# Optimization experiments

Measured on AMD Instinct MI355X. Metric: run time of the kernel, lower is better.

The kernel has to match this reference:

```python
import jax, jax.numpy as jnp
import numpy as np

N = 4096            # number of graph nodes (keypoints)
L_MAX = 6
Q = 2
D, H, W = 64, 128, 128
ST = 0.15           # sigma_transition
SP = 0.3            # sigma_pairwise
AU = 1.0            # alpha_unary
L = len(range(0, 2 * L_MAX + 1, Q)) ** 3   # 343 displacement labels


def setup_inputs() -> dict:
    key = jax.random.key(0)
    k1, k2 = jax.random.split(key)
    unary = jax.random.normal(k1, (N, L), dtype=jnp.float32)
    u = jax.random.uniform(k2, (N, N), dtype=jnp.float32)
    dist = (u + u.T) * 0.5  # symmetric pairwise distance matrix
    # Buffer A exactly as in __init__: displacement grid -> RBF transition kernel
    r = np.arange(0, 2 * L_MAX + 1, Q, dtype=np.float32)
    g = np.stack(np.meshgrid(r, r, r, indexing='ij'), axis=3).reshape(-1, 3) - L_MAX
    disp = g[:, ::-1] * 2.0 / np.array([W - 1, H - 1, D - 1], dtype=np.float32)
    A = np.exp(-((disp[:, None, :] - disp[None, :, :]) ** 2).sum(-1) / (2.0 * ST ** 2))
    return {"unary": unary, "dist": dist, "A": jnp.asarray(A, dtype=jnp.float32)}


def _forward(unary, dist, A):
    n, l = unary.shape
    unary = AU * unary
    pairwise = jnp.exp(-dist / (2.0 * SP ** 2))
    INF = jnp.float32(1e30)
    idx = jnp.arange(n)
    d = dist.at[idx, idx].set(INF)  # no self edges

    # ---- Prim's MST rooted at node 0 (addition order = parents-before-children) ----
    in_tree0 = jnp.zeros((n,), dtype=bool).at[0].set(True)
    best0 = d[0]                      # cheapest edge from each node into the tree
    parent0 = jnp.zeros((n,), jnp.int32)
    order0 = jnp.zeros((n,), jnp.int32)

    def prim_body(i, st):
        in_tree, best, parent, order = st
        nxt = jnp.argmin(jnp.where(in_tree, INF, best)).astype(jnp.int32)
        in_tree = in_tree.at[nxt].set(True)
        order = order.at[i].set(nxt)
        upd = (d[nxt] < best) & ~in_tree
        parent = jnp.where(upd, nxt, parent)
        best = jnp.where(upd, d[nxt], best)
        return (in_tree, best, parent, order)

    _, _, parent, order = jax.lax.fori_loop(1, n, prim_body, (in_tree0, best0, parent0, order0))
    root = order[0]  # == 0

    # ---- Upward (leaves -> root) max-sum Viterbi messages along tree edges ----
    ptr0 = jnp.zeros((n, l), jnp.int32)

    def up(carry, c):
        belief, ptr = carry
        p = parent[c]
        # scores[l_c, l_p] = belief[c, l_c] + pairwise(c,p) * A[l_c, l_p]
        scores = belief[c][:, None] + pairwise[c, p] * A
        msg = scores.max(axis=0)                                   # [L]
        ptr = ptr.at[c].set(jnp.argmax(scores, axis=0).astype(jnp.int32))
        belief = belief.at[p].add(jnp.where(c == root, 0.0, msg))  # root sends nothing
        return (belief, ptr), None

    (belief, ptr), _ = jax.lax.scan(up, (unary, ptr0), order[::-1])

    # ---- Downward backtracking (root -> leaves) ----
    def down(labels, c):
        lab = jnp.where(c == root,
                        jnp.argmax(belief[root]).astype(jnp.int32),
                        ptr[c, labels[parent[c]]])
        return labels.at[c].set(lab), None

    labels, _ = jax.lax.scan(down, jnp.zeros((n,), jnp.int32), order)

    # disp_out = -1 everywhere, +1 at selected label, scaled by 1e5
    onehot = jax.nn.one_hot(labels, l, dtype=unary.dtype)
    return (2.0 * onehot - 1.0) * 100000.0


def reference(unary, dist, A):
    return _forward(unary, dist, A)
```

## Files before the change

### kernel.cpp

```cpp
#include <hip/hip_runtime.h>
#include <hip/hip_cooperative_groups.h>
#include <math.h>

namespace cg = cooperative_groups;
typedef unsigned long long u64;

#define NN 4096
#define LBL 343
#define PSTRIDE 344
#define U64MAX 0xFFFFFFFFFFFFFFFFull
#define MST_ROUNDS 12

__global__ void mrf_mst_init_kernel(int* __restrict__ compA,
                                    u64* __restrict__ minEa, u64* __restrict__ minEb,
                                    int* __restrict__ counters)
{
  const int i = blockIdx.x * blockDim.x + threadIdx.x;
  if (i < NN) { compA[i] = i; minEa[i] = U64MAX; minEb[i] = U64MAX; }
  if (i == 0) { counters[0] = NN; counters[1] = NN; counters[2] = 0; }
}

__global__ __launch_bounds__(1024) void mrf_scan_kernel(
    const float* __restrict__ dist, const int* __restrict__ compR,
    u64* __restrict__ minE, int* __restrict__ counters, int round)
{
  __shared__ int s_cc[16];
  __shared__ u64 s_cv[16];

  if (blockIdx.x == 0 && threadIdx.x == 0) counters[round & 1] = 0;
  if (round > 0 && counters[(round - 1) & 1] <= 1) return;

  const int i    = (blockIdx.x * 1024 + threadIdx.x) >> 6;
  const int lane = threadIdx.x & 63;
  const int wib  = threadIdx.x >> 6;

  const int ci = compR[i];
  const float4* rowp = (const float4*)(dist + (size_t)i * NN);
  const int4* cp = (const int4*)compR;
  u64 best = U64MAX;
  #pragma unroll 4
  for (int k = 0; k < 16; ++k) {
    const int q = k * 64 + lane;
    const float4 dv = rowp[q];
    const int4 cv = cp[q];
    const int j0 = q * 4;
    if (cv.x != ci) { const u64 p = ((u64)__float_as_uint(dv.x) << 24) | ((u64)i << 12) | (u64)(j0    ); best = best < p ? best : p; }
    if (cv.y != ci) { const u64 p = ((u64)__float_as_uint(dv.y) << 24) | ((u64)i << 12) | (u64)(j0 + 1); best = best < p ? best : p; }
    if (cv.z != ci) { const u64 p = ((u64)__float_as_uint(dv.z) << 24) | ((u64)i << 12) | (u64)(j0 + 2); best = best < p ? best : p; }
    if (cv.w != ci) { const u64 p = ((u64)__float_as_uint(dv.w) << 24) | ((u64)i << 12) | (u64)(j0 + 3); best = best < p ? best : p; }
  }
  #pragma unroll
  for (int sh = 32; sh >= 1; sh >>= 1) {
    const u64 o = __shfl_down(best, sh);
    best = best < o ? best : o;
  }
  if (lane == 0) {
    s_cc[wib] = (best == U64MAX) ? -1 : ci;
    s_cv[wib] = best;
  }
  __syncthreads();
  if (threadIdx.x == 0) {
    for (int a = 0; a < 16; ++a) {
      const int c = s_cc[a];
      if (c < 0) continue;
      bool dup = false;
      for (int b2 = 0; b2 < a; ++b2) if (s_cc[b2] == c) { dup = true; break; }
      if (dup) continue;
      u64 b = s_cv[a];
      for (int b2 = a + 1; b2 < 16; ++b2)
        if (s_cc[b2] == c && s_cv[b2] < b) b = s_cv[b2];
      atomicMin(&minE[c & (NN - 1)], b);
    }
  }
}

__global__ __launch_bounds__(1024) void mrf_hook_kernel(
    const int* __restrict__ compR, int* __restrict__ compW,
    const u64* __restrict__ minE, u64* __restrict__ minEnext,
    int* __restrict__ eu, int* __restrict__ ev, unsigned* __restrict__ ew,
    int* __restrict__ counters, int round)
{
  if (round > 0 && counters[(round - 1) & 1] <= 1) return;
  const int i = blockIdx.x * 1024 + threadIdx.x;
  if (i >= NN) return;
  minEnext[i] = U64MAX;

  const int r0 = compR[i];
  int cur = r0;
  for (int guard = 0; guard < NN + 2; ++guard) {
    const u64 e = minE[cur];
    if (e == U64MAX) break;
    const int v = (int)(e & 0xFFF);
    const int t = compR[v];
    if (t == cur) break;
    const u64 te = minE[t];
    if (te != U64MAX) {
      const int tv = (int)(te & 0xFFF);
      if (compR[tv] == cur && cur < t) break;
    }
    cur = t;
  }
  compW[i] = cur;
  if (cur == i) atomicAdd(&counters[round & 1], 1);

  if (r0 == i) {
    const u64 e = minE[i];
    if (e != U64MAX) {
      const int v = (int)(e & 0xFFF);
      const int u = (int)((e >> 12) & 0xFFF);
      const unsigned wb = (unsigned)(e >> 24);
      const int t = compR[v];
      bool mutual = false;
      const u64 te = minE[t];
      if (te != U64MAX) {
        const int tv = (int)(te & 0xFFF);
        mutual = (compR[tv] == i);
      }
      if (!(mutual && i < t)) {
        const int slot = atomicAdd(&counters[2], 1);
        if (slot < NN) { eu[slot] = u; ev[slot] = v; ew[slot] = wb; }
      }
    }
  }
}

__device__ __forceinline__ void scan4096(int* arr, int* tmp16, int tid)
{
  __syncthreads();
  const int base = tid * 4;
  const int c0 = arr[base], c1 = arr[base + 1], c2 = arr[base + 2], c3 = arr[base + 3];
  const int lsum = c0 + c1 + c2 + c3;
  const int lane = tid & 63, wid = tid >> 6;
  int incl = lsum;
  #pragma unroll
  for (int o = 1; o < 64; o <<= 1) {
    const int t = __shfl_up(incl, o);
    if (lane >= o) incl += t;
  }
  if (lane == 63) tmp16[wid] = incl;
  __syncthreads();
  if (tid == 0) {
    int run = 0;
    for (int w = 0; w < 16; ++w) { const int t = tmp16[w]; tmp16[w] = run; run += t; }
  }
  __syncthreads();
  const int excl = tmp16[wid] + incl - lsum;
  arr[base]     = excl;
  arr[base + 1] = excl + c0;
  arr[base + 2] = excl + c0 + c1;
  arr[base + 3] = excl + c0 + c1 + c2;
  __syncthreads();
}

__global__ __launch_bounds__(1024) void mrf_root_kernel(
    const float* __restrict__ dist,
    const int* __restrict__ eu, const int* __restrict__ ev, const unsigned* __restrict__ ew,
    int* __restrict__ parent_g, int* __restrict__ childStart, int* __restrict__ childList,
    int* __restrict__ levStart, int* __restrict__ levNodes, int* __restrict__ segList,
    int* __restrict__ meta, float* __restrict__ w_edge,
    u64* __restrict__ adjList, int* __restrict__ ready)
{
  __shared__ int s_deg[NN];
  __shared__ int s_start[NN];
  __shared__ int s_cur[NN];
  __shared__ int s_parent[NN];
  __shared__ unsigned short s_dep[NN];
  __shared__ unsigned short s_fr[2][NN];
  __shared__ int s_tmp16[16];
  __shared__ int s_fcnt, s_nf;

  const int tid = threadIdx.x;

  for (int j = tid; j < NN; j += 1024) ready[j] = 0;

  for (int j = tid; j < NN; j += 1024) s_deg[j] = 0;
  __syncthreads();
  for (int e = tid; e < NN - 1; e += 1024) {
    atomicAdd(&s_deg[eu[e] & (NN - 1)], 1);
    atomicAdd(&s_deg[ev[e] & (NN - 1)], 1);
  }
  __syncthreads();
  for (int j = tid; j < NN; j += 1024) s_start[j] = s_deg[j];
  scan4096(s_start, s_tmp16, tid);
  for (int j = tid; j < NN; j += 1024) s_cur[j] = s_start[j];
  __syncthreads();
  for (int e = tid; e < NN - 1; e += 1024) {
    const int u = eu[e] & (NN - 1), v = ev[e] & (NN - 1);
    const u64 wb = (u64)ew[e];
    const int p1 = atomicAdd(&s_cur[u], 1);
    adjList[p1] = (wb << 12) | (u64)v;
    const int p2 = atomicAdd(&s_cur[v], 1);
    adjList[p2] = (wb << 12) | (u64)u;
  }
  __syncthreads();

  for (int j = tid; j < NN; j += 1024) { s_parent[j] = 0; s_dep[j] = 0; }
  if (tid == 0) { s_fcnt = 1; s_nf = 0; s_fr[0][0] = 0; }
  __syncthreads();
  int cur = 0, lev = 0;
  while (true) {
    const int fcnt = s_fcnt;
    if (fcnt == 0) break;
    for (int idx = tid; idx < fcnt; idx += 1024) {
      const int x = s_fr[cur][idx];
      const int st = s_start[x], dg = s_deg[x];
      for (int a = 0; a < dg; ++a) {
        const u64 ent = adjList[st + a];
        const int nb = (int)(ent & 0xFFF);
        if (nb != s_parent[x] || x == 0) {
          s_parent[nb] = x;
          s_dep[nb] = (unsigned short)(lev + 1);
          const int slot = atomicAdd(&s_nf, 1);
          s_fr[1 - cur][slot] = (unsigned short)nb;
        }
      }
    }
    __syncthreads();
    if (tid == 0) { s_fcnt = s_nf; s_nf = 0; }
    ++lev;
    cur ^= 1;
    __syncthreads();
  }
  const int numLev = lev;
  if (tid == 0) { s_parent[0] = 0; meta[0] = numLev; }
  __syncthreads();

  int* s_cs2 = (int*)s_fr;
  for (int j = tid; j < NN; j += 1024) s_cs2[j] = s_deg[j] - (j != 0 ? 1 : 0);
  scan4096(s_cs2, s_tmp16, tid);
  for (int j = tid; j < NN; j += 1024) childStart[j] = s_cs2[j];
  if (tid == 0) childStart[NN] = NN - 1;
  __syncthreads();

  for (int p = tid; p < NN; p += 1024) {
    const int st = s_start[p], dg = s_deg[p], cs = s_cs2[p];
    const int par = s_parent[p];
    u64 buf[16];
    int m = 0;
    for (int a = 0; a < dg; ++a) {
      const u64 ent = adjList[st + a];
      const int nb = (int)(ent & 0xFFF);
      if (p != 0 && nb == par) continue;
      if (m < 16) {
        int q = m;
        while (q > 0 && buf[q - 1] < ent) { buf[q] = buf[q - 1]; --q; }
        buf[q] = ent;
        ++m;
      } else {
        childList[cs + m] = nb;
        ++m;
      }
    }
    const int lim = m < 16 ? m : 16;
    for (int k = 0; k < lim; ++k) childList[cs + k] = (int)(buf[k] & 0xFFF);
  }

  for (int j = tid; j < NN; j += 1024) s_cur[j] = 0;
  __syncthreads();
  for (int j = tid; j < NN; j += 1024) atomicAdd(&s_cur[s_dep[j]], 1);
  scan4096(s_cur, s_tmp16, tid);
  for (int j = tid; j < NN; j += 1024) { levStart[j] = s_cur[j]; s_start[j] = s_cur[j]; }
  if (tid == 0) levStart[NN] = NN;
  __syncthreads();
  for (int j = tid; j < NN; j += 1024) {
    const int pos = atomicAdd(&s_start[s_dep[j]], 1);
    levNodes[pos] = j;
  }
  __syncthreads();

  if (tid == 0) s_nf = 0;
  for (int j = tid; j < NN; j += 1024) s_cur[j] = 0;
  __syncthreads();
  for (int j = tid; j < NN; j += 1024) {
    const int ce = (j == NN - 1) ? (NN - 1) : s_cs2[j + 1];
    int key = -1;
    if (ce - s_cs2[j] == 0) {
      int c = j;
      while (c != 0) {
        const int par = s_parent[c];
        if (childList[s_cs2[par]] != c) break;
        c = par;
      }
      key = s_dep[c];
      atomicAdd(&s_cur[numLev - 1 - key], 1);
      atomicAdd(&s_nf, 1);
    }
    s_deg[j] = key;
  }
  scan4096(s_cur, s_tmp16, tid);
  for (int j = tid; j < NN; j += 1024) s_start[j] = s_cur[j];
  __syncthreads();
  for (int j = tid; j < NN; j += 1024) {
    const int key = s_deg[j];
    if (key >= 0) {
      const int pos = atomicAdd(&s_start[numLev - 1 - key], 1);
      segList[pos] = j;
    }
  }
  if (tid == 0) meta[1] = s_nf;

  for (int j = tid; j < NN; j += 1024) {
    parent_g[j] = s_parent[j];
    w_edge[j] = (j == 0) ? 0.0f
                         : expf(-dist[(size_t)j * NN + s_parent[j]] / 0.18f);
  }
}

__global__ __launch_bounds__(768) void mrf_solve_kernel(
    const float* __restrict__ unary, const float* __restrict__ A,
    float* __restrict__ msgbuf, unsigned short* __restrict__ ptrbuf,
    const int* __restrict__ parent, const int* __restrict__ childStart,
    const int* __restrict__ childList, const int* __restrict__ levStart,
    const int* __restrict__ levNodes, const int* __restrict__ segList,
    const float* __restrict__ w_edge,
    int* __restrict__ labels, const int* __restrict__ meta,
    int* __restrict__ ready)
{
  __shared__ float s_b[LBL];
  __shared__ int s_lab[NN];
  __shared__ float s_pv[2][384];
  __shared__ int   s_pi[2][384];
  const int tid = threadIdx.x;
  const int h   = (tid >= 384) ? 1 : 0;
  const int lp  = tid - h * 384;
  const int lc0 = h ? 172 : 0;
  const int lc1 = h ? LBL : 172;

  int numLev = meta[0];
  if (numLev < 1) numLev = 1;
  if (numLev > NN) numLev = NN;
  int numSegs = meta[1];
  if (numSegs < 1) numSegs = 1;
  if (numSegs > NN) numSegs = NN;

  bool didRoot = false;

  for (int sidx = blockIdx.x; sidx < numSegs && !didRoot; sidx += gridDim.x) {
    int v = segList[sidx] & (NN - 1);
    float b = (tid < LBL) ? unary[(size_t)v * LBL + tid] : 0.0f;

    while (true) {
      if (tid < LBL) s_b[tid] = b;
      __syncthreads();

      if (v == 0) {
        if (tid == 0) {
          float bv = s_b[0]; int bi = 0;
          for (int l = 1; l < LBL; ++l)
            if (s_b[l] > bv) { bv = s_b[l]; bi = l; }
          labels[0] = bi;
          s_lab[0] = bi;
        }
        __syncthreads();
        didRoot = true;
        break;
      }

      {
        float bv = 0.0f; int bi = lc0;
        if (lp < LBL) {
          const float w = w_edge[v];
          const float* __restrict__ Ac = A + lp;
          bv = __fadd_rn(s_b[lc0], __fmul_rn(w, Ac[(size_t)lc0 * LBL]));
          int lc = lc0 + 1;
          for (; ((lc1 - lc) & 7) != 0; ++lc) {
            const float s = __fadd_rn(s_b[lc], __fmul_rn(w, Ac[(size_t)lc * LBL]));
            if (s > bv) { bv = s; bi = lc; }
          }
          for (; lc < lc1; lc += 8) {
            const float a0 = Ac[(size_t)(lc + 0) * LBL];
            const float a1 = Ac[(size_t)(lc + 1) * LBL];
            const float a2 = Ac[(size_t)(lc + 2) * LBL];
            const float a3 = Ac[(size_t)(lc + 3) * LBL];
            const float a4 = Ac[(size_t)(lc + 4) * LBL];
            const float a5 = Ac[(size_t)(lc + 5) * LBL];
            const float a6 = Ac[(size_t)(lc + 6) * LBL];
            const float a7 = Ac[(size_t)(lc + 7) * LBL];
            const float s0 = __fadd_rn(s_b[lc + 0], __fmul_rn(w, a0));
            const float s1 = __fadd_rn(s_b[lc + 1], __fmul_rn(w, a1));
            const float s2 = __fadd_rn(s_b[lc + 2], __fmul_rn(w, a2));
            const float s3 = __fadd_rn(s_b[lc + 3], __fmul_rn(w, a3));
            const float s4 = __fadd_rn(s_b[lc + 4], __fmul_rn(w, a4));
            const float s5 = __fadd_rn(s_b[lc + 5], __fmul_rn(w, a5));
            const float s6 = __fadd_rn(s_b[lc + 6], __fmul_rn(w, a6));
            const float s7 = __fadd_rn(s_b[lc + 7], __fmul_rn(w, a7));
            if (s0 > bv) { bv = s0; bi = lc + 0; }
            if (s1 > bv) { bv = s1; bi = lc + 1; }
            if (s2 > bv) { bv = s2; bi = lc + 2; }
            if (s3 > bv) { bv = s3; bi = lc + 3; }
            if (s4 > bv) { bv = s4; bi = lc + 4; }
            if (s5 > bv) { bv = s5; bi = lc + 5; }
            if (s6 > bv) { bv = s6; bi = lc + 6; }
            if (s7 > bv) { bv = s7; bi = lc + 7; }
          }
        }
        s_pv[h][lp] = bv;
        s_pi[h][lp] = bi;
      }
      __syncthreads();

      float fbv = 0.0f; int fbi = 0;
      if (tid < LBL) {
        fbv = s_pv[0][tid]; fbi = s_pi[0][tid];
        const float v1 = s_pv[1][tid];
        if (v1 > fbv) { fbv = v1; fbi = s_pi[1][tid]; }
      }
      const int nbi = __shfl_down(fbi, 1);
      if (tid < LBL && (tid & 1) == 0) {
        const unsigned pk = ((unsigned)fbi & 0xFFFFu) | (((unsigned)nbi & 0xFFFFu) << 16);
        __hip_atomic_store((unsigned*)(ptrbuf + (size_t)v * PSTRIDE + tid), pk,
                           __ATOMIC_RELAXED, __HIP_MEMORY_SCOPE_AGENT);
      }

      const int p = parent[v] & (NN - 1);
      const int csp = childStart[p];
      int degp = childStart[p + 1] - csp;
      if (degp < 1) degp = 1;
      if (degp > 64) degp = 64;
      const bool isCarrier = ((childList[csp] & (NN - 1)) == v);

      if (!isCarrier) {
        if (tid < LBL)
          __hip_atomic_store((unsigned*)&msgbuf[(size_t)v * LBL + tid],
                             __float_as_uint(fbv),
                             __ATOMIC_RELAXED, __HIP_MEMORY_SCOPE_AGENT);
        __syncthreads();
        if (tid == 0)
          __hip_atomic_fetch_add(&ready[p], 1,
                                 __ATOMIC_RELEASE, __HIP_MEMORY_SCOPE_AGENT);
        break;
      }

      if (degp > 1 && tid == 0) {
        long long guard = 0;
        while (__hip_atomic_load(&ready[p], __ATOMIC_RELAXED,
                                 __HIP_MEMORY_SCOPE_AGENT) < degp - 1) {
          __builtin_amdgcn_s_sleep(1);
          if (++guard > 30000000LL) break;
        }
      }
      __syncthreads();

      if (tid < LBL) {
        float nb = __fadd_rn(unary[(size_t)p * LBL + tid], fbv);
        for (int k = 1; k < degp; ++k) {
          const int ch = childList[csp + k] & (NN - 1);
          const unsigned um = __hip_atomic_load(
              (const unsigned*)&msgbuf[(size_t)ch * LBL + tid],
              __ATOMIC_RELAXED, __HIP_MEMORY_SCOPE_AGENT);
          nb = __fadd_rn(nb, __uint_as_float(um));
        }
        b = nb;
      }
      v = p;
    }
  }

  if (!didRoot) return;
  __syncthreads();
  for (int lev = 1; lev < numLev; ++lev) {
    int ls = levStart[lev], le = levStart[lev + 1];
    if (ls < 0) ls = 0;
    if (le > NN) le = NN;
    for (int idx = ls + tid; idx < le; idx += 768) {
      const int c = levNodes[idx] & (NN - 1);
      int pl = s_lab[parent[c] & (NN - 1)];
      if (pl < 0) pl = 0;
      if (pl >= LBL) pl = LBL - 1;
      const unsigned pk = __hip_atomic_load(
          (const unsigned*)(ptrbuf + (size_t)c * PSTRIDE + (pl & ~1)),
          __ATOMIC_RELAXED, __HIP_MEMORY_SCOPE_AGENT);
      const int lab = (pl & 1) ? (int)(pk >> 16) : (int)(pk & 0xFFFFu);
      s_lab[c] = lab;
      labels[c] = lab;
    }
    __syncthreads();
  }
}

__global__ void mrf_out_kernel(const int* __restrict__ labels, float* __restrict__ out)
{
  const int id = blockIdx.x * blockDim.x + threadIdx.x;
  if (id >= NN * LBL) return;
  const int c = id / LBL;
  const int l = id - c * LBL;
  out[id] = (l == labels[c]) ? 100000.0f : -100000.0f;
}

extern "C" void kernel_launch(void* const* d_in, const int* in_sizes, int n_in,
                              void* d_out, int out_size, void* d_ws, size_t ws_size,
                              hipStream_t stream)
{
  (void)in_sizes; (void)n_in; (void)out_size; (void)ws_size;
  const float* unary = (const float*)d_in[0];
  const float* dist  = (const float*)d_in[1];
  const float* A     = (const float*)d_in[2];
  float* out = (float*)d_out;

  char* ws = (char*)d_ws;
  size_t off = 0;
  auto take = [&](size_t bytes) -> void* {
    void* p = (void*)(ws + off);
    off += (bytes + 255) & ~(size_t)255;
    return p;
  };
  float* msgbuf = out;
  unsigned short* ptrbuf = (unsigned short*)take((size_t)NN * PSTRIDE * sizeof(unsigned short));
  int*      compA      = (int*)     take(NN * sizeof(int));
  int*      compB      = (int*)     take(NN * sizeof(int));
  u64*      minEa      = (u64*)     take(NN * sizeof(u64));
  u64*      minEb      = (u64*)     take(NN * sizeof(u64));
  int*      eu         = (int*)     take(NN * sizeof(int));
  int*      ev         = (int*)     take(NN * sizeof(int));
  unsigned* ew         = (unsigned*)take(NN * sizeof(unsigned));
  int*      counters   = (int*)     take(256);
  int*      parent     = (int*)     take(NN * sizeof(int));
  int*      childStart = (int*)     take((NN + 1) * sizeof(int));
  int*      childList  = (int*)     take(NN * sizeof(int));
  int*      levStart   = (int*)     take((NN + 1) * sizeof(int));
  int*      levNodes   = (int*)     take(NN * sizeof(int));
  int*      segList    = (int*)     take(NN * sizeof(int));
  int*      labels     = (int*)     take(NN * sizeof(int));
  int*      meta       = (int*)     take(256);
  float*    w_edge     = (float*)   take(NN * sizeof(float));
  int*      ready      = (int*)     take(NN * sizeof(int));
  u64*      adjList    = (u64*)     take((size_t)2 * NN * sizeof(u64));

  hipLaunchKernelGGL(mrf_mst_init_kernel, dim3(4), dim3(1024), 0, stream,
                     compA, minEa, minEb, counters);

  for (int r = 0; r < MST_ROUNDS; ++r) {
    const int* compR = (r & 1) ? compB : compA;
    int*       compW = (r & 1) ? compA : compB;
    u64*       mcur  = (r & 1) ? minEb : minEa;
    u64*       mnext = (r & 1) ? minEa : minEb;
    hipLaunchKernelGGL(mrf_scan_kernel, dim3(256), dim3(1024), 0, stream,
                       dist, compR, mcur, counters, r);
    hipLaunchKernelGGL(mrf_hook_kernel, dim3(4), dim3(1024), 0, stream,
                       compR, compW, mcur, mnext, eu, ev, ew, counters, r);
  }

  hipLaunchKernelGGL(mrf_root_kernel, dim3(1), dim3(1024), 0, stream,
                     dist, eu, ev, ew, parent, childStart, childList,
                     levStart, levNodes, segList, meta, w_edge, adjList, ready);

  {
    void* args[] = {
      (void*)&unary, (void*)&A, (void*)&msgbuf, (void*)&ptrbuf,
      (void*)&parent, (void*)&childStart, (void*)&childList,
      (void*)&levStart, (void*)&levNodes, (void*)&segList, (void*)&w_edge,
      (void*)&labels, (void*)&meta, (void*)&ready
    };
    hipLaunchCooperativeKernel((void*)mrf_solve_kernel, dim3(256), dim3(768),
                               args, 0, stream);
  }

  const int total = NN * LBL;
  hipLaunchKernelGGL(mrf_out_kernel, dim3((total + 255) / 256), dim3(256), 0, stream,
                     labels, out);
}
```

Measured before the change: 980.9 us.

## Drop argmax pointers in upward pass; recompute argmax from stored beliefs during backtrack

The upward message pass now computes only the max, using fmaxf reductions, and stops tracking argmax indices and writing the packed pointer table. Each node's belief vector is saved to a workspace buffer instead. The downward backtracking then recomputes argmax over child labels for the chosen parent label, one wavefront per node with a shuffle reduction that breaks ties toward the lower index. This shortens the serial critical path of the upward pass, at the cost of extra work and global belief reads in the level-by-level backtrack.

```diff
diff --git a/kernel.cpp b/kernel.cpp
--- a/kernel.cpp
+++ b/kernel.cpp
@@ -7,7 +7,6 @@
 
 #define NN 4096
 #define LBL 343
-#define PSTRIDE 344
 #define U64MAX 0xFFFFFFFFFFFFFFFFull
 #define MST_ROUNDS 12
 
@@ -308,7 +307,7 @@
 
 __global__ __launch_bounds__(768) void mrf_solve_kernel(
     const float* __restrict__ unary, const float* __restrict__ A,
-    float* __restrict__ msgbuf, unsigned short* __restrict__ ptrbuf,
+    float* __restrict__ msgbuf, float* __restrict__ belief,
     const int* __restrict__ parent, const int* __restrict__ childStart,
     const int* __restrict__ childList, const int* __restrict__ levStart,
     const int* __restrict__ levNodes, const int* __restrict__ segList,
@@ -319,7 +318,6 @@
   __shared__ float s_b[LBL];
   __shared__ int s_lab[NN];
   __shared__ float s_pv[2][384];
-  __shared__ int   s_pi[2][384];
   const int tid = threadIdx.x;
   const int h   = (tid >= 384) ? 1 : 0;
   const int lp  = tid - h * 384;
@@ -340,7 +338,12 @@
     float b = (tid < LBL) ? unary[(size_t)v * LBL + tid] : 0.0f;
 
     while (true) {
-      if (tid < LBL) s_b[tid] = b;
+      if (tid < LBL) {
+        s_b[tid] = b;
+        __hip_atomic_store((unsigned*)&belief[(size_t)v * LBL + tid],
+                           __float_as_uint(b),
+                           __ATOMIC_RELAXED, __HIP_MEMORY_SCOPE_AGENT);
+      }
       __syncthreads();
 
       if (v == 0) {
@@ -357,7 +360,7 @@
       }
 
       {
-        float bv = 0.0f; int bi = lc0;
+        float bv = 0.0f;
         if (lp < LBL) {
           const float w = w_edge[v];
           const float* __restrict__ Ac = A + lp;
@@ -365,7 +368,7 @@
           int lc = lc0 + 1;
           for (; ((lc1 - lc) & 7) != 0; ++lc) {
             const float s = __fadd_rn(s_b[lc], __fmul_rn(w, Ac[(size_t)lc * LBL]));
-            if (s > bv) { bv = s; bi = lc; }
+            bv = fmaxf(bv, s);
           }
           for (; lc < lc1; lc += 8) {
             const float a0 = Ac[(size_t)(lc + 0) * LBL];
@@ -384,33 +387,19 @@
             const float s5 = __fadd_rn(s_b[lc + 5], __fmul_rn(w, a5));
             const float s6 = __fadd_rn(s_b[lc + 6], __fmul_rn(w, a6));
             const float s7 = __fadd_rn(s_b[lc + 7], __fmul_rn(w, a7));
-            if (s0 > bv) { bv = s0; bi = lc + 0; }
-            if (s1 > bv) { bv = s1; bi = lc + 1; }
-            if (s2 > bv) { bv = s2; bi = lc + 2; }
-            if (s3 > bv) { bv = s3; bi = lc + 3; }
-            if (s4 > bv) { bv = s4; bi = lc + 4; }
-            if (s5 > bv) { bv = s5; bi = lc + 5; }
-            if (s6 > bv) { bv = s6; bi = lc + 6; }
-            if (s7 > bv) { bv = s7; bi = lc + 7; }
+            const float m01 = fmaxf(s0, s1);
+            const float m23 = fmaxf(s2, s3);
+            const float m45 = fmaxf(s4, s5);
+            const float m67 = fmaxf(s6, s7);
+            bv = fmaxf(bv, fmaxf(fmaxf(m01, m23), fmaxf(m45, m67)));
           }
         }
         s_pv[h][lp] = bv;
-        s_pi[h][lp] = bi;
       }
       __syncthreads();
 
-      float fbv = 0.0f; int fbi = 0;
-      if (tid < LBL) {
-        fbv = s_pv[0][tid]; fbi = s_pi[0][tid];
-        const float v1 = s_pv[1][tid];
-        if (v1 > fbv) { fbv = v1; fbi = s_pi[1][tid]; }
-      }
-      const int nbi = __shfl_down(fbi, 1);
-      if (tid < LBL && (tid & 1) == 0) {
-        const unsigned pk = ((unsigned)fbi & 0xFFFFu) | (((unsigned)nbi & 0xFFFFu) << 16);
-        __hip_atomic_store((unsigned*)(ptrbuf + (size_t)v * PSTRIDE + tid), pk,
-                           __ATOMIC_RELAXED, __HIP_MEMORY_SCOPE_AGENT);
-      }
+      float fbv = 0.0f;
+      if (tid < LBL) fbv = fmaxf(s_pv[0][tid], s_pv[1][tid]);
 
       const int p = parent[v] & (NN - 1);
       const int csp = childStart[p];
@@ -458,21 +447,37 @@
 
   if (!didRoot) return;
   __syncthreads();
+  const int wv   = tid >> 6;
+  const int lane = tid & 63;
   for (int lev = 1; lev < numLev; ++lev) {
     int ls = levStart[lev], le = levStart[lev + 1];
     if (ls < 0) ls = 0;
     if (le > NN) le = NN;
-    for (int idx = ls + tid; idx < le; idx += 768) {
+    for (int idx = ls + wv; idx < le; idx += 12) {
       const int c = levNodes[idx] & (NN - 1);
       int pl = s_lab[parent[c] & (NN - 1)];
       if (pl < 0) pl = 0;
       if (pl >= LBL) pl = LBL - 1;
-      const unsigned pk = __hip_atomic_load(
-          (const unsigned*)(ptrbuf + (size_t)c * PSTRIDE + (pl & ~1)),
-          __ATOMIC_RELAXED, __HIP_MEMORY_SCOPE_AGENT);
-      const int lab = (pl & 1) ? (int)(pk >> 16) : (int)(pk & 0xFFFFu);
-      s_lab[c] = lab;
-      labels[c] = lab;
+      const float w = w_edge[c];
+      const float* __restrict__ Arow = A + (size_t)pl * LBL;
+      float bv = -3.4e38f; int bi = 0x3FFFFFFF;
+      for (int lc = lane; lc < LBL; lc += 64) {
+        const unsigned ub = __hip_atomic_load(
+            (const unsigned*)&belief[(size_t)c * LBL + lc],
+            __ATOMIC_RELAXED, __HIP_MEMORY_SCOPE_AGENT);
+        const float s = __fadd_rn(__uint_as_float(ub), __fmul_rn(w, Arow[lc]));
+        if (s > bv) { bv = s; bi = lc; }
+      }
+      #pragma unroll
+      for (int sh = 32; sh >= 1; sh >>= 1) {
+        const float ov = __shfl_down(bv, sh);
+        const int   oi = __shfl_down(bi, sh);
+        if (ov > bv || (ov == bv && oi < bi)) { bv = ov; bi = oi; }
+      }
+      if (lane == 0) {
+        s_lab[c] = bi;
+        labels[c] = bi;
+      }
     }
     __syncthreads();
   }
@@ -505,7 +510,7 @@
     return p;
   };
   float* msgbuf = out;
-  unsigned short* ptrbuf = (unsigned short*)take((size_t)NN * PSTRIDE * sizeof(unsigned short));
+  float*    belief     = (float*)   take((size_t)NN * LBL * sizeof(float));
   int*      compA      = (int*)     take(NN * sizeof(int));
   int*      compB      = (int*)     take(NN * sizeof(int));
   u64*      minEa      = (u64*)     take(NN * sizeof(u64));
@@ -546,7 +551,7 @@
 
   {
     void* args[] = {
-      (void*)&unary, (void*)&A, (void*)&msgbuf, (void*)&ptrbuf,
+      (void*)&unary, (void*)&A, (void*)&msgbuf, (void*)&belief,
       (void*)&parent, (void*)&childStart, (void*)&childList,
       (void*)&levStart, (void*)&levNodes, (void*)&segList, (void*)&w_edge,
       (void*)&labels, (void*)&meta, (void*)&ready
```

Measured after the change: 1.875 ms. 91.2% more time.

## Pad A to float4 pitch and split child labels eight ways

Applied to the files above, without the earlier changes.

Adds a kernel that copies A into a row-padded buffer (pitch 344) so the solve kernel can read four parent labels per thread with float4 loads. Each thread now handles 4 parent labels over 1/8 of the child labels instead of 1 label over half, with an 8-way shared-memory reduction followed by a separate packing pass. Beliefs are kept in shared memory, not registers. This is meant to cut global load instructions and shorten the serial per-node chain along the tree, at the cost of an extra launch, more shared memory and an extra __syncthreads per step.

```diff
diff --git a/kernel.cpp b/kernel.cpp
--- a/kernel.cpp
+++ b/kernel.cpp
@@ -8,6 +8,7 @@
 #define NN 4096
 #define LBL 343
 #define PSTRIDE 344
+#define APITCH 344
 #define U64MAX 0xFFFFFFFFFFFFFFFFull
 #define MST_ROUNDS 12
 
@@ -18,6 +19,15 @@
   const int i = blockIdx.x * blockDim.x + threadIdx.x;
   if (i < NN) { compA[i] = i; minEa[i] = U64MAX; minEb[i] = U64MAX; }
   if (i == 0) { counters[0] = NN; counters[1] = NN; counters[2] = 0; }
+}
+
+__global__ void mrf_padA_kernel(const float* __restrict__ A, float* __restrict__ Apad)
+{
+  const int id = blockIdx.x * 256 + threadIdx.x;
+  if (id >= LBL * APITCH) return;
+  const int r = id / APITCH;
+  const int c = id - r * APITCH;
+  Apad[id] = (c < LBL) ? A[r * LBL + c] : 0.0f;
 }
 
 __global__ __launch_bounds__(1024) void mrf_scan_kernel(
@@ -307,7 +317,7 @@
 }
 
 __global__ __launch_bounds__(768) void mrf_solve_kernel(
-    const float* __restrict__ unary, const float* __restrict__ A,
+    const float* __restrict__ unary, const float* __restrict__ Apad,
     float* __restrict__ msgbuf, unsigned short* __restrict__ ptrbuf,
     const int* __restrict__ parent, const int* __restrict__ childStart,
     const int* __restrict__ childList, const int* __restrict__ levStart,
@@ -316,15 +326,16 @@
     int* __restrict__ labels, const int* __restrict__ meta,
     int* __restrict__ ready)
 {
-  __shared__ float s_b[LBL];
-  __shared__ int s_lab[NN];
-  __shared__ float s_pv[2][384];
-  __shared__ int   s_pi[2][384];
+  __shared__ float s_b[APITCH];
+  __shared__ float s_pv[8][APITCH];
+  __shared__ int   s_pi[8][APITCH];
+  __shared__ int   s_lab[NN];
   const int tid = threadIdx.x;
-  const int h   = (tid >= 384) ? 1 : 0;
-  const int lp  = tid - h * 384;
-  const int lc0 = h ? 172 : 0;
-  const int lc1 = h ? LBL : 172;
+  const bool act = (tid < 688);
+  const int t = act ? (tid % 86) : 0;
+  const int h = act ? (tid / 86) : 0;
+  const int lc0 = h * 43;
+  const int lc1 = (h == 7) ? LBL : (lc0 + 43);
 
   int numLev = meta[0];
   if (numLev < 1) numLev = 1;
@@ -337,12 +348,10 @@
 
   for (int sidx = blockIdx.x; sidx < numSegs && !didRoot; sidx += gridDim.x) {
     int v = segList[sidx] & (NN - 1);
-    float b = (tid < LBL) ? unary[(size_t)v * LBL + tid] : 0.0f;
+    if (tid < LBL) s_b[tid] = unary[(size_t)v * LBL + tid];
+    __syncthreads();
 
     while (true) {
-      if (tid < LBL) s_b[tid] = b;
-      __syncthreads();
-
       if (v == 0) {
         if (tid == 0) {
           float bv = s_b[0]; int bi = 0;
@@ -356,59 +365,56 @@
         break;
       }
 
-      {
-        float bv = 0.0f; int bi = lc0;
-        if (lp < LBL) {
-          const float w = w_edge[v];
-          const float* __restrict__ Ac = A + lp;
-          bv = __fadd_rn(s_b[lc0], __fmul_rn(w, Ac[(size_t)lc0 * LBL]));
-          int lc = lc0 + 1;
-          for (; ((lc1 - lc) & 7) != 0; ++lc) {
-            const float s = __fadd_rn(s_b[lc], __fmul_rn(w, Ac[(size_t)lc * LBL]));
-            if (s > bv) { bv = s; bi = lc; }
-          }
-          for (; lc < lc1; lc += 8) {
-            const float a0 = Ac[(size_t)(lc + 0) * LBL];
-            const float a1 = Ac[(size_t)(lc + 1) * LBL];
-            const float a2 = Ac[(size_t)(lc + 2) * LBL];
-            const float a3 = Ac[(size_t)(lc + 3) * LBL];
-            const float a4 = Ac[(size_t)(lc + 4) * LBL];
-            const float a5 = Ac[(size_t)(lc + 5) * LBL];
-            const float a6 = Ac[(size_t)(lc + 6) * LBL];
-            const float a7 = Ac[(size_t)(lc + 7) * LBL];
-            const float s0 = __fadd_rn(s_b[lc + 0], __fmul_rn(w, a0));
-            const float s1 = __fadd_rn(s_b[lc + 1], __fmul_rn(w, a1));
-            const float s2 = __fadd_rn(s_b[lc + 2], __fmul_rn(w, a2));
-            const float s3 = __fadd_rn(s_b[lc + 3], __fmul_rn(w, a3));
-            const float s4 = __fadd_rn(s_b[lc + 4], __fmul_rn(w, a4));
-            const float s5 = __fadd_rn(s_b[lc + 5], __fmul_rn(w, a5));
-            const float s6 = __fadd_rn(s_b[lc + 6], __fmul_rn(w, a6));
-            const float s7 = __fadd_rn(s_b[lc + 7], __fmul_rn(w, a7));
-            if (s0 > bv) { bv = s0; bi = lc + 0; }
-            if (s1 > bv) { bv = s1; bi = lc + 1; }
-            if (s2 > bv) { bv = s2; bi = lc + 2; }
-            if (s3 > bv) { bv = s3; bi = lc + 3; }
-            if (s4 > bv) { bv = s4; bi = lc + 4; }
-            if (s5 > bv) { bv = s5; bi = lc + 5; }
-            if (s6 > bv) { bv = s6; bi = lc + 6; }
-            if (s7 > bv) { bv = s7; bi = lc + 7; }
-          }
+      if (act) {
+        const float w = w_edge[v];
+        const float4* __restrict__ Ap4 = (const float4*)Apad;
+        float4 a = Ap4[(size_t)lc0 * 86 + t];
+        float sb = s_b[lc0];
+        float bv0 = __fadd_rn(sb, __fmul_rn(w, a.x));
+        float bv1 = __fadd_rn(sb, __fmul_rn(w, a.y));
+        float bv2 = __fadd_rn(sb, __fmul_rn(w, a.z));
+        float bv3 = __fadd_rn(sb, __fmul_rn(w, a.w));
+        int bi0 = lc0, bi1 = lc0, bi2 = lc0, bi3 = lc0;
+        #pragma unroll 2
+        for (int lc = lc0 + 1; lc < lc1; ++lc) {
+          const float4 av = Ap4[(size_t)lc * 86 + t];
+          const float sbl = s_b[lc];
+          const float s0 = __fadd_rn(sbl, __fmul_rn(w, av.x));
+          const float s1 = __fadd_rn(sbl, __fmul_rn(w, av.y));
+          const float s2 = __fadd_rn(sbl, __fmul_rn(w, av.z));
+          const float s3 = __fadd_rn(sbl, __fmul_rn(w, av.w));
+          if (s0 > bv0) { bv0 = s0; bi0 = lc; }
+          if (s1 > bv1) { bv1 = s1; bi1 = lc; }
+          if (s2 > bv2) { bv2 = s2; bi2 = lc; }
+          if (s3 > bv3) { bv3 = s3; bi3 = lc; }
         }
-        s_pv[h][lp] = bv;
-        s_pi[h][lp] = bi;
+        const int lpb = t * 4;
+        s_pv[h][lpb + 0] = bv0; s_pi[h][lpb + 0] = bi0;
+        s_pv[h][lpb + 1] = bv1; s_pi[h][lpb + 1] = bi1;
+        s_pv[h][lpb + 2] = bv2; s_pi[h][lpb + 2] = bi2;
+        s_pv[h][lpb + 3] = bv3; s_pi[h][lpb + 3] = bi3;
       }
       __syncthreads();
 
-      float fbv = 0.0f; int fbi = 0;
+      float fbv = 0.0f;
       if (tid < LBL) {
-        fbv = s_pv[0][tid]; fbi = s_pi[0][tid];
-        const float v1 = s_pv[1][tid];
-        if (v1 > fbv) { fbv = v1; fbi = s_pi[1][tid]; }
-      }
-      const int nbi = __shfl_down(fbi, 1);
-      if (tid < LBL && (tid & 1) == 0) {
-        const unsigned pk = ((unsigned)fbi & 0xFFFFu) | (((unsigned)nbi & 0xFFFFu) << 16);
-        __hip_atomic_store((unsigned*)(ptrbuf + (size_t)v * PSTRIDE + tid), pk,
+        fbv = s_pv[0][tid];
+        int fbi = s_pi[0][tid];
+        #pragma unroll
+        for (int hh = 1; hh < 8; ++hh) {
+          const float pv = s_pv[hh][tid];
+          if (pv > fbv) { fbv = pv; fbi = s_pi[hh][tid]; }
+        }
+        s_pi[0][tid] = fbi;
+      }
+      __syncthreads();
+
+      if (tid < 172) {
+        const unsigned lo = (unsigned)s_pi[0][2 * tid] & 0xFFFFu;
+        const unsigned hi = (2 * tid + 1 < LBL)
+                              ? ((unsigned)s_pi[0][2 * tid + 1] & 0xFFFFu) : 0u;
+        __hip_atomic_store((unsigned*)(ptrbuf + (size_t)v * PSTRIDE + 2 * tid),
+                           lo | (hi << 16),
                            __ATOMIC_RELAXED, __HIP_MEMORY_SCOPE_AGENT);
       }
 
@@ -450,9 +456,10 @@
               __ATOMIC_RELAXED, __HIP_MEMORY_SCOPE_AGENT);
           nb = __fadd_rn(nb, __uint_as_float(um));
         }
-        b = nb;
+        s_b[tid] = nb;
       }
       v = p;
+      __syncthreads();
     }
   }
 
@@ -506,6 +513,7 @@
   };
   float* msgbuf = out;
   unsigned short* ptrbuf = (unsigned short*)take((size_t)NN * PSTRIDE * sizeof(unsigned short));
+  float*    Apad       = (float*)   take((size_t)LBL * APITCH * sizeof(float));
   int*      compA      = (int*)     take(NN * sizeof(int));
   int*      compB      = (int*)     take(NN * sizeof(int));
   u64*      minEa      = (u64*)     take(NN * sizeof(u64));
@@ -528,6 +536,8 @@
 
   hipLaunchKernelGGL(mrf_mst_init_kernel, dim3(4), dim3(1024), 0, stream,
                      compA, minEa, minEb, counters);
+  hipLaunchKernelGGL(mrf_padA_kernel, dim3((LBL * APITCH + 255) / 256), dim3(256),
+                     0, stream, A, Apad);
 
   for (int r = 0; r < MST_ROUNDS; ++r) {
     const int* compR = (r & 1) ? compB : compA;
@@ -546,7 +556,7 @@
 
   {
     void* args[] = {
-      (void*)&unary, (void*)&A, (void*)&msgbuf, (void*)&ptrbuf,
+      (void*)&unary, (void*)&Apad, (void*)&msgbuf, (void*)&ptrbuf,
       (void*)&parent, (void*)&childStart, (void*)&childList,
       (void*)&levStart, (void*)&levNodes, (void*)&segList, (void*)&w_edge,
       (void*)&labels, (void*)&meta, (void*)&ready
```

New measurement: 907.9 us. -7.4%, faster.
